# Optimization experiments

Hardware: AMD Instinct MI355X
Metric: run time of the kernel (lower is better)

The kernel has to match this reference:

```python
import jax, jax.numpy as jnp
import numpy as np

EMBED_DIM = 512
NUM_NEURONS = 4096
B, T = 8, 2048
# get_tide_level(birth_epoch=1) = 0.05 + (0.8-0.05)*(1/600)
INIT_SCALE = 0.05 + (0.8 - 0.05) * (1.0 / 600.0)


def setup_inputs() -> dict:
    key = jax.random.key(0)
    kx, kp, kv, kt = jax.random.split(key, 4)
    x = jax.random.normal(kx, (B, T, EMBED_DIM), dtype=jnp.float32)
    positions = jax.random.normal(kp, (NUM_NEURONS, EMBED_DIM), dtype=jnp.float32) * 0.5
    values = jax.random.normal(kv, (NUM_NEURONS, EMBED_DIM), dtype=jnp.float32) * 0.02
    temperature = jnp.full((NUM_NEURONS,), 0.5, dtype=jnp.float32)
    neuron_scale = jnp.full((NUM_NEURONS,), INIT_SCALE, dtype=jnp.float32)
    return {"x": x, "positions": positions, "values": values,
            "temperature": temperature, "neuron_scale": neuron_scale}


def reference(x, positions, values, temperature, neuron_scale):
    Bv, Tv, D = x.shape
    x_flat = x.reshape(-1, D)                                  # [M, D]
    # Euclidean cdist via the expansion trick (matmul-dominant)
    x2 = jnp.sum(x_flat * x_flat, axis=-1, keepdims=True)      # [M, 1]
    p2 = jnp.sum(positions * positions, axis=-1)               # [N]
    d2 = x2 + p2[None, :] - 2.0 * (x_flat @ positions.T)       # [M, N]
    dists = jnp.sqrt(jnp.maximum(d2, 0.0))
    effective_temp = (jnp.abs(temperature) + 0.1) * neuron_scale  # [N]
    weights = jnp.exp(-dists / effective_temp[None, :])        # [M, N]
    weights = weights / (jnp.sum(weights, axis=-1, keepdims=True) + 1e-8)
    out = weights @ values                                     # [M, D]
    return out.reshape(Bv, Tv, D)
```

## Files before the change

### kernel.cpp

```cpp
#include <hip/hip_runtime.h>
#include <hip/hip_fp16.h>


typedef _Float16 f16;
typedef _Float16 f16x8 __attribute__((ext_vector_type(8)));
typedef float f32x4 __attribute__((ext_vector_type(4)));
typedef int i32x4 __attribute__((ext_vector_type(4)));
typedef unsigned char u8;
typedef unsigned int u32;

#define DEV __device__ __forceinline__

DEV void gload16(const void* g, void* l) {
  __builtin_amdgcn_global_load_lds(
      (const __attribute__((address_space(1))) void*)g,
      (__attribute__((address_space(3))) void*)l, 16, 0, 0);
}

DEV int pack4_fp8(float a, float b, float c, float d) {
  int lo = __builtin_amdgcn_cvt_pk_fp8_f32(a, b, 0, false);
  int hi = __builtin_amdgcn_cvt_pk_fp8_f32(c, d, 0, false);
  return (hi << 16) | (lo & 0xffff);
}


DEV void row_pack(const float* __restrict__ src, u8* __restrict__ dst,
                  float* __restrict__ sq, int blk) {
  int row  = blk * 4 + (threadIdx.x >> 6);
  int lane = threadIdx.x & 63;
  const float* r = src + (size_t)row * 512 + lane * 8;
  float4 a = *(const float4*)r;
  float4 b = *(const float4*)(r + 4);
  int2 pk;
  pk.x = pack4_fp8(a.x, a.y, a.z, a.w);
  pk.y = pack4_fp8(b.x, b.y, b.z, b.w);
  *(int2*)(dst + (size_t)row * 512 + lane * 8) = pk;
  float ss = a.x*a.x + a.y*a.y + a.z*a.z + a.w*a.w
           + b.x*b.x + b.y*b.y + b.z*b.z + b.w*b.w;
  ss += __shfl_xor(ss, 1);  ss += __shfl_xor(ss, 2);  ss += __shfl_xor(ss, 4);
  ss += __shfl_xor(ss, 8);  ss += __shfl_xor(ss, 16); ss += __shfl_xor(ss, 32);
  if (lane == 0) sq[row] = ss;
}

__global__ __launch_bounds__(256) void prep_all(
    const float* __restrict__ x, const float* __restrict__ pos,
    const float* __restrict__ val, const float* __restrict__ T,
    const float* __restrict__ ns,
    u8* __restrict__ X8, u8* __restrict__ P8, u8* __restrict__ Vt8,
    float* __restrict__ x2, float* __restrict__ p2,
    float* __restrict__ invt) {
  __shared__ f16 Tt[64][72];
  int b = blockIdx.x;
  if (b < 4096) {
    row_pack(x, X8, x2, b);
  } else if (b < 5120) {
    row_pack(pos, P8, p2, b - 4096);
  } else if (b < 5632) {
    int id = b - 5120;
    int n0 = (id & 63) * 64, d0 = (id >> 6) * 64;
    int t = threadIdx.x;
#pragma unroll
    for (int rr = 0; rr < 4; ++rr) {
      int r  = (t >> 4) + rr * 16;
      int cq = t & 15;
      float4 v = *(const float4*)(val + (size_t)(n0 + r) * 512 + d0 + cq * 4);
      Tt[cq*4+0][r] = (f16)v.x; Tt[cq*4+1][r] = (f16)v.y;
      Tt[cq*4+2][r] = (f16)v.z; Tt[cq*4+3][r] = (f16)v.w;
    }
    __syncthreads();
    int rd = t >> 2, part = t & 3;
    int p4 = part * 4;
    i32x4 pk;
    pk.x = pack4_fp8((float)Tt[rd][p4+0], (float)Tt[rd][16+p4+0],
                     (float)Tt[rd][32+p4+0], (float)Tt[rd][48+p4+0]);
    pk.y = pack4_fp8((float)Tt[rd][p4+1], (float)Tt[rd][16+p4+1],
                     (float)Tt[rd][32+p4+1], (float)Tt[rd][48+p4+1]);
    pk.z = pack4_fp8((float)Tt[rd][p4+2], (float)Tt[rd][16+p4+2],
                     (float)Tt[rd][32+p4+2], (float)Tt[rd][48+p4+2]);
    pk.w = pack4_fp8((float)Tt[rd][p4+3], (float)Tt[rd][16+p4+3],
                     (float)Tt[rd][32+p4+3], (float)Tt[rd][48+p4+3]);
    *(i32x4*)(Vt8 + (size_t)(d0 + rd) * 4096 + n0 + part * 16) = pk;
  } else {
    int i = (b - 5632) * 256 + threadIdx.x;
    invt[i] = 1.0f / ((fabsf(T[i]) + 0.1f) * ns[i]);
  }
}

__global__ __launch_bounds__(64) void bounds_k(
    const float* __restrict__ x2, const float* __restrict__ p2,
    const float* __restrict__ invt, float* __restrict__ xb,
    float* __restrict__ nb) {
  int t = threadIdx.x;
  float lo, hi;
  if (blockIdx.x < 128) {
    int base = blockIdx.x * 128;
    float a = __builtin_amdgcn_sqrtf(x2[base + t]);
    float b = __builtin_amdgcn_sqrtf(x2[base + 64 + t]);
    lo = fminf(a, b); hi = fmaxf(a, b);
  } else {
    int base = (blockIdx.x - 128) * 128;
    float pa = __builtin_amdgcn_sqrtf(p2[base + t]);
    float pb = __builtin_amdgcn_sqrtf(p2[base + 64 + t]);
    float ra = 112.0f / invt[base + t];
    float rb = 112.0f / invt[base + 64 + t];
    lo = fminf(pa - ra, pb - rb); hi = fmaxf(pa + ra, pb + rb);
  }
#pragma unroll
  for (int s = 1; s < 64; s <<= 1) {
    lo = fminf(lo, __shfl_xor(lo, s));
    hi = fmaxf(hi, __shfl_xor(hi, s));
  }
  if (t == 0) {
    if (blockIdx.x < 128) { xb[blockIdx.x*2] = lo; xb[blockIdx.x*2+1] = hi; }
    else { int i = blockIdx.x - 128; nb[i*2] = lo; nb[i*2+1] = hi; }
  }
}

template <int EPI>
__global__ __launch_bounds__(256, 2) void gemm_bt(
    const void* __restrict__ A, const void* __restrict__ B, int Kb, int gx,
    const float* __restrict__ x2, const float* __restrict__ p2,
    const float* __restrict__ invt, u8* __restrict__ Wout,
    float* __restrict__ Wpart, void* __restrict__ flagsp,
    const float* __restrict__ xb, const float* __restrict__ nb,
    const float* __restrict__ rowsum, float* __restrict__ outp) {
  __shared__ __align__(16) char smem[65536];
  char* As = smem;
  char* Bs = smem + 16384;

  const int nwg = gridDim.x;
  const int sid = (blockIdx.x & 7) * (nwg >> 3) + (blockIdx.x >> 3);
  const int bx = sid % gx, by = sid / gx;

  const int tid = threadIdx.x, lane = tid & 63, w = tid >> 6;
  const int wrow = (w >> 1) * 64, wcol = (w & 1) * 64;
  const int g = lane >> 4, r15 = lane & 15;
  const int m0 = by * 128;

  const char* Ablk = (const char*)A + (size_t)m0 * Kb;

  const int lr = lane >> 3;
  const int lo = (lane & 7) ^ lr;
  const char* aSrc[4]; char* aDst[4]; char* bDst[4];
  int srow[4];
#pragma unroll
  for (int i = 0; i < 4; ++i) {
    int cb  = w * 4 + i;
    srow[i] = cb * 8 + lr;
    aSrc[i] = Ablk + (size_t)srow[i] * Kb + 16 * lo;
    aDst[i] = As + cb * 1024;
    bDst[i] = Bs + cb * 1024;
  }

  int abase[4], asw[4], bbase[4], bsw[4];
#pragma unroll
  for (int mt = 0; mt < 4; ++mt) {
    int r = wrow + mt * 16 + r15;
    abase[mt] = r * 128; asw[mt] = (r & 7) << 4;
    int rb = wcol + mt * 16 + r15;
    bbase[mt] = rb * 128; bsw[mt] = (rb & 7) << 4;
  }

  const int NIT = Kb >> 7;
  constexpr int nrep = (EPI == 0) ? 4 : 1;
  const u32* fl = (const u32*)flagsp;

  if constexpr (EPI == 1) {
    if (fl[bx * 32] != 0) {
      const char* Bblk0 = (const char*)B + (size_t)(bx * nrep * 128) * Kb;
#pragma unroll
      for (int i = 0; i < 4; ++i) gload16(aSrc[i], aDst[i]);
#pragma unroll
      for (int i = 0; i < 4; ++i)
        gload16(Bblk0 + (size_t)srow[i] * Kb + 16 * lo, bDst[i]);
    }
  }

  float xlo, xhi;
  if constexpr (EPI == 0) { xlo = xb[by * 2]; xhi = xb[by * 2 + 1]; }

  for (int j = 0; j < nrep; ++j) {
    const int bxj = bx * nrep + j;
    const int n0 = bxj * 128;

    if constexpr (EPI == 0) {
      float blo = nb[bxj * 2], bhi = nb[bxj * 2 + 1];
      if (xhi < blo || xlo > bhi) {
        if (lane == 0)
          ((u8*)flagsp)[(size_t)(by * 32 + bxj) * 4 + w] = 0;
        int r = tid >> 1, half = tid & 1;
        Wpart[(size_t)(m0 + r) * 64 + bxj * 2 + half] = 0.0f;
        continue;
      }
    }

    const char* Bblk = (const char*)B + (size_t)n0 * Kb;
    const char* bSrc[4];
#pragma unroll
    for (int i = 0; i < 4; ++i)
      bSrc[i] = Bblk + (size_t)srow[i] * Kb + 16 * lo;

    __syncthreads();
    if constexpr (EPI == 0) {
#pragma unroll
      for (int i = 0; i < 4; ++i) gload16(aSrc[i], aDst[i]);
#pragma unroll
      for (int i = 0; i < 4; ++i) gload16(bSrc[i], bDst[i]);
      __syncthreads();
    }
    f32x4 acc[4][4] = {};

#pragma unroll 2
    for (int it = 0; it < NIT; ++it) {
      const int cur = (it & 1) << 15;
      const int nxt = cur ^ 32768;
      bool fnx = true, fcu = true;
      if constexpr (EPI == 1) {
        fcu = fl[bx * 32 + it] != 0;
        if (it + 1 < NIT) fnx = fl[bx * 32 + it + 1] != 0;
      }
      if (it + 1 < NIT && fnx) {
        const int kb1 = (it + 1) << 7;
#pragma unroll
        for (int i = 0; i < 4; ++i) gload16(aSrc[i] + kb1, aDst[i] + nxt);
#pragma unroll
        for (int i = 0; i < 4; ++i) gload16(bSrc[i] + kb1, bDst[i] + nxt);
      }
      if (fcu) {
        const char* As_ = As + cur;
        const char* Bs_ = Bs + cur;
#pragma unroll
        for (int ks = 0; ks < 4; ++ks) {
          long aL[4], bL[4];
#pragma unroll
          for (int mt = 0; mt < 4; ++mt)
            aL[mt] = *(const long*)(As_ + (abase[mt] + ((32 * ks + 8 * g) ^ asw[mt])));
#pragma unroll
          for (int nt = 0; nt < 4; ++nt)
            bL[nt] = *(const long*)(Bs_ + (bbase[nt] + ((32 * ks + 8 * g) ^ bsw[nt])));
#pragma unroll
          for (int mt = 0; mt < 4; ++mt)
#pragma unroll
            for (int nt = 0; nt < 4; ++nt)
              acc[mt][nt] = __builtin_amdgcn_mfma_f32_16x16x32_fp8_fp8(aL[mt], bL[nt],
                                                                       acc[mt][nt], 0, 0, 0);
        }
      }
      __syncthreads();
    }

    if constexpr (EPI == 0) {
      float* Ws = (float*)(smem + 32768);
      float p2v[4], itv[4], thr[4];
#pragma unroll
      for (int nt = 0; nt < 4; ++nt) {
        int n = n0 + wcol + nt * 16 + r15;
        p2v[nt] = p2[n]; itv[nt] = invt[n];
        float lim = 104.0f / itv[nt];
        thr[nt] = lim * lim;
      }
      u8* wbase = Wout + n0 + wcol + 4 * r15;
      bool tnz = false;
#pragma unroll
      for (int mt = 0; mt < 4; ++mt) {
#pragma unroll
        for (int reg = 0; reg < 4; ++reg) {
          int ml = wrow + mt * 16 + g * 4 + reg;
          float xx = x2[m0 + ml];
          float d20 = xx + p2v[0] - 2.0f * acc[mt][0][reg];
          float d21 = xx + p2v[1] - 2.0f * acc[mt][1][reg];
          float d22 = xx + p2v[2] - 2.0f * acc[mt][2][reg];
          float d23 = xx + p2v[3] - 2.0f * acc[mt][3][reg];
          int dw = 0;
          float s = 0.0f;
          bool pred = (d20 < thr[0]) || (d21 < thr[1]) ||
                      (d22 < thr[2]) || (d23 < thr[3]);
          if (__any(pred)) {
            float wv0 = __expf(-__builtin_amdgcn_sqrtf(fmaxf(d20, 0.0f)) * itv[0]);
            float wv1 = __expf(-__builtin_amdgcn_sqrtf(fmaxf(d21, 0.0f)) * itv[1]);
            float wv2 = __expf(-__builtin_amdgcn_sqrtf(fmaxf(d22, 0.0f)) * itv[2]);
            float wv3 = __expf(-__builtin_amdgcn_sqrtf(fmaxf(d23, 0.0f)) * itv[3]);
            dw = pack4_fp8(wv0, wv1, wv2, wv3);
            s = wv0 + wv1 + wv2 + wv3;
            tnz = tnz || (dw != 0);
          }
          __builtin_nontemporal_store(dw, (int*)(wbase + (size_t)(m0 + ml) * 4096));
          Ws[ml * 36 + (w & 1) * 16 + r15] = s;
        }
      }
      {
        bool wnz = __any(tnz);
        if (lane == 0)
          ((u8*)flagsp)[(size_t)(by * 32 + bxj) * 4 + w] = wnz ? 1 : 0;
      }
      __syncthreads();
      {
        int r = tid >> 1, half = tid & 1;
        const float* sp = Ws + r * 36 + half * 16;
        float4 a0 = *(const float4*)(sp);
        float4 a1 = *(const float4*)(sp + 4);
        float4 a2 = *(const float4*)(sp + 8);
        float4 a3 = *(const float4*)(sp + 12);
        float s = a0.x+a0.y+a0.z+a0.w + a1.x+a1.y+a1.z+a1.w
                + a2.x+a2.y+a2.z+a2.w + a3.x+a3.y+a3.z+a3.w;
        Wpart[(size_t)(m0 + r) * 64 + bxj * 2 + half] = s;
      }
    } else {
      float* Tb = (float*)(smem) + w * (32 * 66);
      const int dl = lane & 31, half = lane >> 5;
#pragma unroll
      for (int h = 0; h < 2; ++h) {
#pragma unroll
        for (int mh = 0; mh < 2; ++mh) {
          int mt = h * 2 + mh;
#pragma unroll
          for (int nt = 0; nt < 4; ++nt)
#pragma unroll
            for (int reg = 0; reg < 4; ++reg)
              Tb[(mh * 16 + g * 4 + reg) * 66 + nt * 16 + r15] = acc[mt][nt][reg];
        }
#pragma unroll
        for (int rr = 0; rr < 32; ++rr) {
          int mloc = rr * 2 + half;
          float v = Tb[dl * 66 + mloc];
          int mg = n0 + wcol + mloc;
          int dg = m0 + wrow + h * 32 + dl;
          float nrm = 1.0f / (rowsum[mg] + 1e-8f);
          __builtin_nontemporal_store(v * nrm, &outp[(size_t)mg * 512 + dg]);
        }
        __syncthreads();
      }
    }
  }
}

__global__ __launch_bounds__(256) void rowsum_k(const float* __restrict__ Wpart,
                                                float* __restrict__ rowsum) {
  int row  = blockIdx.x * 4 + (threadIdx.x >> 6);
  int lane = threadIdx.x & 63;
  float v = Wpart[(size_t)row * 64 + lane];
  v += __shfl_xor(v, 1);  v += __shfl_xor(v, 2);  v += __shfl_xor(v, 4);
  v += __shfl_xor(v, 8);  v += __shfl_xor(v, 16); v += __shfl_xor(v, 32);
  if (lane == 0) rowsum[row] = v;
}


extern "C" void kernel_launch(void* const* d_in, const int* in_sizes, int n_in,
                              void* d_out, int out_size, void* d_ws, size_t ws_size,
                              hipStream_t stream) {
  const float* x   = (const float*)d_in[0];
  const float* pos = (const float*)d_in[1];
  const float* val = (const float*)d_in[2];
  const float* tmp = (const float*)d_in[3];
  const float* nsc = (const float*)d_in[4];
  float* out = (float*)d_out;

  char* p = (char*)d_ws;
  u8*    X8     = (u8*)p;    p += (size_t)16384 * 512;
  u8*    P8     = (u8*)p;    p += (size_t)4096 * 512;
  u8*    Vt8    = (u8*)p;    p += (size_t)512 * 4096;
  float* x2     = (float*)p; p += (size_t)16384 * 4;
  float* p2     = (float*)p; p += (size_t)4096 * 4;
  float* invt   = (float*)p; p += (size_t)4096 * 4;
  float* rowsum = (float*)p; p += (size_t)16384 * 4;
  float* Wpart  = (float*)p; p += (size_t)16384 * 64 * 4;
  void*  flags  = (void*)p;  p += (size_t)128 * 32 * 4;
  float* xb     = (float*)p; p += (size_t)128 * 2 * 4;
  float* nb     = (float*)p; p += (size_t)32 * 2 * 4;
  u8*    W8     = (u8*)p;
  size_t fixed  = (size_t)(p - (char*)d_ws);
  size_t wfull  = (size_t)16384 * 4096;

  if (fixed + wfull > ws_size) return;

  prep_all<<<5648, 256, 0, stream>>>(x, pos, val, tmp, nsc,
                                     X8, P8, Vt8, x2, p2, invt);
  bounds_k<<<160, 64, 0, stream>>>(x2, p2, invt, xb, nb);

  gemm_bt<0><<<8 * 128, 256, 0, stream>>>(
      X8, P8, 512, 8, x2, p2, invt, W8, Wpart, flags, xb, nb,
      nullptr, nullptr);
  rowsum_k<<<4096, 256, 0, stream>>>(Wpart, rowsum);
  gemm_bt<1><<<128 * 4, 256, 0, stream>>>(
      Vt8, W8, 4096, 128, nullptr, nullptr, nullptr, nullptr, nullptr, flags,
      nullptr, nullptr, rowsum, out);
}
```

Measured before the change: 40.16 us.

## Fuse row-sum reduction into second GEMM and skip all-zero tiles early

Removes the separate rowsum kernel launch. Each block of the second GEMM now reduces its 128 rows of Wpart into shared memory before it starts the main loop. It also checks all 32 K-tile flags with a wave vote and skips the whole MFMA loop, including its barriers, when every tile is zero. This saves one launch and a global round trip for rowsum. In exchange, four blocks that share the same bx each redo the same row reduction, and an extra barrier runs at block start.

```diff
diff --git a/kernel.cpp b/kernel.cpp
--- a/kernel.cpp
+++ b/kernel.cpp
@@ -123,7 +123,7 @@
     const float* __restrict__ invt, u8* __restrict__ Wout,
     float* __restrict__ Wpart, void* __restrict__ flagsp,
     const float* __restrict__ xb, const float* __restrict__ nb,
-    const float* __restrict__ rowsum, float* __restrict__ outp) {
+    float* __restrict__ outp) {
   __shared__ __align__(16) char smem[65536];
   char* As = smem;
   char* Bs = smem + 16384;
@@ -165,9 +165,29 @@
   constexpr int nrep = (EPI == 0) ? 4 : 1;
   const u32* fl = (const u32*)flagsp;
 
+  float* rsum = (float*)(smem + 40960);
+  bool anyNZ = true;
   if constexpr (EPI == 1) {
-    if (fl[bx * 32] != 0) {
-      const char* Bblk0 = (const char*)B + (size_t)(bx * nrep * 128) * Kb;
+    {
+      int r = tid >> 1, half = tid & 1;
+      const float* wp = Wpart + (size_t)(bx * 128 + r) * 64 + half;
+      float v = 0.f;
+#pragma unroll
+      for (int t2 = 0; t2 < 32; ++t2) v += wp[t2 * 2];
+      v += __shfl_xor(v, 1);
+      if (half == 0) rsum[r] = v;
+    }
+    u32 f = (lane < 32) ? fl[bx * 32 + lane] : 0;
+    anyNZ = __any(f != 0);
+    __syncthreads();
+  }
+
+  float xlo, xhi;
+  if constexpr (EPI == 0) { xlo = xb[by * 2]; xhi = xb[by * 2 + 1]; }
+
+  if constexpr (EPI == 1) {
+    if (anyNZ && fl[bx * 32] != 0) {
+      const char* Bblk0 = (const char*)B + (size_t)(bx * 128) * Kb;
 #pragma unroll
       for (int i = 0; i < 4; ++i) gload16(aSrc[i], aDst[i]);
 #pragma unroll
@@ -175,9 +195,6 @@
         gload16(Bblk0 + (size_t)srow[i] * Kb + 16 * lo, bDst[i]);
     }
   }
-
-  float xlo, xhi;
-  if constexpr (EPI == 0) { xlo = xb[by * 2]; xhi = xb[by * 2 + 1]; }
 
   for (int j = 0; j < nrep; ++j) {
     const int bxj = bx * nrep + j;
@@ -194,59 +211,64 @@
       }
     }
 
-    const char* Bblk = (const char*)B + (size_t)n0 * Kb;
-    const char* bSrc[4];
-#pragma unroll
-    for (int i = 0; i < 4; ++i)
-      bSrc[i] = Bblk + (size_t)srow[i] * Kb + 16 * lo;
-
-    __syncthreads();
-    if constexpr (EPI == 0) {
-#pragma unroll
-      for (int i = 0; i < 4; ++i) gload16(aSrc[i], aDst[i]);
-#pragma unroll
-      for (int i = 0; i < 4; ++i) gload16(bSrc[i], bDst[i]);
+    f32x4 acc[4][4] = {};
+    bool dense = true;
+    if constexpr (EPI == 1) dense = anyNZ;
+
+    if (dense) {
+      const char* Bblk = (const char*)B + (size_t)n0 * Kb;
+      const char* bSrc[4];
+#pragma unroll
+      for (int i = 0; i < 4; ++i)
+        bSrc[i] = Bblk + (size_t)srow[i] * Kb + 16 * lo;
+
       __syncthreads();
-    }
-    f32x4 acc[4][4] = {};
+      if constexpr (EPI == 0) {
+#pragma unroll
+        for (int i = 0; i < 4; ++i) gload16(aSrc[i], aDst[i]);
+#pragma unroll
+        for (int i = 0; i < 4; ++i) gload16(bSrc[i], bDst[i]);
+        __syncthreads();
+      }
 
 #pragma unroll 2
-    for (int it = 0; it < NIT; ++it) {
-      const int cur = (it & 1) << 15;
-      const int nxt = cur ^ 32768;
-      bool fnx = true, fcu = true;
-      if constexpr (EPI == 1) {
-        fcu = fl[bx * 32 + it] != 0;
-        if (it + 1 < NIT) fnx = fl[bx * 32 + it + 1] != 0;
-      }
-      if (it + 1 < NIT && fnx) {
-        const int kb1 = (it + 1) << 7;
-#pragma unroll
-        for (int i = 0; i < 4; ++i) gload16(aSrc[i] + kb1, aDst[i] + nxt);
-#pragma unroll
-        for (int i = 0; i < 4; ++i) gload16(bSrc[i] + kb1, bDst[i] + nxt);
-      }
-      if (fcu) {
-        const char* As_ = As + cur;
-        const char* Bs_ = Bs + cur;
-#pragma unroll
-        for (int ks = 0; ks < 4; ++ks) {
-          long aL[4], bL[4];
-#pragma unroll
-          for (int mt = 0; mt < 4; ++mt)
-            aL[mt] = *(const long*)(As_ + (abase[mt] + ((32 * ks + 8 * g) ^ asw[mt])));
-#pragma unroll
-          for (int nt = 0; nt < 4; ++nt)
-            bL[nt] = *(const long*)(Bs_ + (bbase[nt] + ((32 * ks + 8 * g) ^ bsw[nt])));
-#pragma unroll
-          for (int mt = 0; mt < 4; ++mt)
+      for (int it = 0; it < NIT; ++it) {
+        const int cur = (it & 1) << 15;
+        const int nxt = cur ^ 32768;
+        bool fnx = true, fcu = true;
+        if constexpr (EPI == 1) {
+          fcu = fl[bx * 32 + it] != 0;
+          if (it + 1 < NIT) fnx = fl[bx * 32 + it + 1] != 0;
+        }
+        if (it + 1 < NIT && fnx) {
+          const int kb1 = (it + 1) << 7;
+#pragma unroll
+          for (int i = 0; i < 4; ++i) gload16(aSrc[i] + kb1, aDst[i] + nxt);
+#pragma unroll
+          for (int i = 0; i < 4; ++i) gload16(bSrc[i] + kb1, bDst[i] + nxt);
+        }
+        if (fcu) {
+          const char* As_ = As + cur;
+          const char* Bs_ = Bs + cur;
+#pragma unroll
+          for (int ks = 0; ks < 4; ++ks) {
+            long aL[4], bL[4];
+#pragma unroll
+            for (int mt = 0; mt < 4; ++mt)
+              aL[mt] = *(const long*)(As_ + (abase[mt] + ((32 * ks + 8 * g) ^ asw[mt])));
 #pragma unroll
             for (int nt = 0; nt < 4; ++nt)
-              acc[mt][nt] = __builtin_amdgcn_mfma_f32_16x16x32_fp8_fp8(aL[mt], bL[nt],
-                                                                       acc[mt][nt], 0, 0, 0);
-        }
-      }
-      __syncthreads();
+              bL[nt] = *(const long*)(Bs_ + (bbase[nt] + ((32 * ks + 8 * g) ^ bsw[nt])));
+#pragma unroll
+            for (int mt = 0; mt < 4; ++mt)
+#pragma unroll
+              for (int nt = 0; nt < 4; ++nt)
+                acc[mt][nt] = __builtin_amdgcn_mfma_f32_16x16x32_fp8_fp8(aL[mt], bL[nt],
+                                                                         acc[mt][nt], 0, 0, 0);
+          }
+        }
+        __syncthreads();
+      }
     }
 
     if constexpr (EPI == 0) {
@@ -325,23 +347,13 @@
           float v = Tb[dl * 66 + mloc];
           int mg = n0 + wcol + mloc;
           int dg = m0 + wrow + h * 32 + dl;
-          float nrm = 1.0f / (rowsum[mg] + 1e-8f);
+          float nrm = 1.0f / (rsum[wcol + mloc] + 1e-8f);
           __builtin_nontemporal_store(v * nrm, &outp[(size_t)mg * 512 + dg]);
         }
         __syncthreads();
       }
     }
   }
-}
-
-__global__ __launch_bounds__(256) void rowsum_k(const float* __restrict__ Wpart,
-                                                float* __restrict__ rowsum) {
-  int row  = blockIdx.x * 4 + (threadIdx.x >> 6);
-  int lane = threadIdx.x & 63;
-  float v = Wpart[(size_t)row * 64 + lane];
-  v += __shfl_xor(v, 1);  v += __shfl_xor(v, 2);  v += __shfl_xor(v, 4);
-  v += __shfl_xor(v, 8);  v += __shfl_xor(v, 16); v += __shfl_xor(v, 32);
-  if (lane == 0) rowsum[row] = v;
 }
 
 
@@ -362,7 +374,6 @@
   float* x2     = (float*)p; p += (size_t)16384 * 4;
   float* p2     = (float*)p; p += (size_t)4096 * 4;
   float* invt   = (float*)p; p += (size_t)4096 * 4;
-  float* rowsum = (float*)p; p += (size_t)16384 * 4;
   float* Wpart  = (float*)p; p += (size_t)16384 * 64 * 4;
   void*  flags  = (void*)p;  p += (size_t)128 * 32 * 4;
   float* xb     = (float*)p; p += (size_t)128 * 2 * 4;
@@ -378,10 +389,8 @@
   bounds_k<<<160, 64, 0, stream>>>(x2, p2, invt, xb, nb);
 
   gemm_bt<0><<<8 * 128, 256, 0, stream>>>(
-      X8, P8, 512, 8, x2, p2, invt, W8, Wpart, flags, xb, nb,
-      nullptr, nullptr);
-  rowsum_k<<<4096, 256, 0, stream>>>(Wpart, rowsum);
+      X8, P8, 512, 8, x2, p2, invt, W8, Wpart, flags, xb, nb, nullptr);
   gemm_bt<1><<<128 * 4, 256, 0, stream>>>(
-      Vt8, W8, 4096, 128, nullptr, nullptr, nullptr, nullptr, nullptr, flags,
-      nullptr, nullptr, rowsum, out);
-}
+      Vt8, W8, 4096, 128, nullptr, nullptr, nullptr, nullptr, Wpart, flags,
+      nullptr, nullptr, out);
+}
```

After: 38.61 us. 3.9% less time.
